# Kernel tuning notes

Hardware: AMD Instinct MI355X
Metric: run time of the kernel (lower is better)

Reference implementation:

```python
import jax, jax.numpy as jnp
import numpy as np

NUM_ITERATIONS = 100
EPS = 1e-6
LIPSCHITZ_COEFF = 0.9


def _l2_normalize(x, axis=None, eps=1e-12):
    return x * jax.lax.rsqrt((x * x).sum(axis=axis, keepdims=True) + eps)


def setup_inputs() -> dict:
    key = jax.random.key(0)
    k1, k2, k3, k4 = jax.random.split(key, 4)
    B, D_in, D_out = 32768, 1024, 1024
    x = jax.random.normal(k1, (B, D_in), dtype=jnp.float32)
    # TruncatedNormal(stddev=1/sqrt(fan_in)) approximated by scaled normal
    w = jax.random.normal(k2, (D_in, D_out), dtype=jnp.float32) / np.sqrt(D_in)
    b = jax.random.normal(k3, (D_out,), dtype=jnp.float32)
    u0 = jax.random.normal(k4, (1, D_out), dtype=jnp.float32)
    return {"x": x, "w": w, "b": b, "u0": u0}


def reference(x, w, b, u0):
    d_in = w.shape[0]

    # 100-step power iteration: tight sequential dependency chain of GEMV pairs.
    def body(i, carry):
        u, _ = carry
        v = _l2_normalize(jnp.matmul(u, w.T), eps=EPS)   # [1, d_in]
        u = _l2_normalize(jnp.matmul(v, w), eps=EPS)     # [1, d_out]
        return (u, v)

    v_init = jnp.zeros((1, d_in), dtype=w.dtype)
    u, v = jax.lax.fori_loop(0, NUM_ITERATIONS, body, (u0, v_init))
    u = jax.lax.stop_gradient(u)
    v = jax.lax.stop_gradient(v)

    sigma = jnp.matmul(jnp.matmul(v, w), u.T)[0, 0]      # spectral norm estimate
    factor = jnp.maximum(1.0, sigma / LIPSCHITZ_COEFF)
    w_norm = w / factor

    out = jnp.dot(x, w_norm) + b
    return out
```

## Files before the change

kernel.cpp:

```cpp
#include <hip/hip_runtime.h>
#include <hip/hip_bf16.h>
#include <cstdint>
#include <cstddef>

#define DDIM 1024
#define BROWS 32768

typedef __attribute__((ext_vector_type(8))) short short8;
typedef __attribute__((ext_vector_type(4))) float floatx4;

__device__ __forceinline__ float bf2f(unsigned short u) {
  return __uint_as_float(((unsigned int)u) << 16);
}
__device__ __forceinline__ unsigned short f2bf(float f) {
  unsigned int u = __float_as_uint(f);
  u += 0x7FFFu + ((u >> 16) & 1u);
  return (unsigned short)(u >> 16);
}

__device__ __forceinline__ void load_lds16(const void* g, void* l) {
  __builtin_amdgcn_global_load_lds(
      (const __attribute__((address_space(1))) unsigned int*)g,
      (__attribute__((address_space(3))) unsigned int*)l,
      16, 0, 0);
}

__global__ void __launch_bounds__(256, 2)
big_gemm(const float* __restrict__ Af, const unsigned short* __restrict__ Bt,
         float* __restrict__ Outf, const float* __restrict__ inv_ptr,
         const float* __restrict__ bias)
{
  __shared__ unsigned short As[128 * 32];
  __shared__ unsigned short Bs[128 * 32];

  const int tid  = threadIdx.x;
  const int lane = tid & 63;
  const int wid  = tid >> 6;
  const int wr = wid >> 1, wc = wid & 1;
  const int g = lane >> 4, r = lane & 15;

  const int bm0 = (int)(blockIdx.x & 255) * 128;
  const int bn0 = (int)(blockIdx.x >> 8) * 128;

  const floatx4 zero4 = {0.f, 0.f, 0.f, 0.f};
  floatx4 acc[4][4];
#pragma unroll
  for (int m = 0; m < 4; ++m)
#pragma unroll
    for (int n = 0; n < 4; ++n) acc[m][n] = zero4;

  for (int kk = 0; kk < DDIM; kk += 32) {
    __syncthreads();
#pragma unroll
    for (int p = 0; p < 2; ++p) {
      const int o = p * 4096 + tid * 16;
      const int row = o >> 6;
      const int cole = (o & 63) >> 1;
      load_lds16(Bt + (size_t)(bn0 + row) * DDIM + kk + cole, (char*)Bs + o);
    }
#pragma unroll
    for (int p = 0; p < 2; ++p) {
      const int o = p * 4096 + tid * 16;
      const int row = o >> 6;
      const int cole = (o & 63) >> 1;
      const float4* s = (const float4*)(Af + (size_t)(bm0 + row) * DDIM + kk + cole);
      float4 x0 = s[0], x1 = s[1];
      short8 t;
      t[0] = (short)f2bf(x0.x); t[1] = (short)f2bf(x0.y);
      t[2] = (short)f2bf(x0.z); t[3] = (short)f2bf(x0.w);
      t[4] = (short)f2bf(x1.x); t[5] = (short)f2bf(x1.y);
      t[6] = (short)f2bf(x1.z); t[7] = (short)f2bf(x1.w);
      *(short8*)((char*)As + o) = t;
    }
    __syncthreads();

    short8 afr[4], bfr[4];
#pragma unroll
    for (int m = 0; m < 4; ++m)
      afr[m] = *(const short8*)((const char*)As + (wr * 64 + m * 16 + r) * 64 + g * 16);
#pragma unroll
    for (int n = 0; n < 4; ++n)
      bfr[n] = *(const short8*)((const char*)Bs + (wc * 64 + n * 16 + r) * 64 + g * 16);
#pragma unroll
    for (int m = 0; m < 4; ++m)
#pragma unroll
      for (int n = 0; n < 4; ++n)
        acc[m][n] = __builtin_amdgcn_mfma_f32_16x16x32_bf16(afr[m], bfr[n], acc[m][n], 0, 0, 0);
  }

  const float inv = *inv_ptr;
#pragma unroll
  for (int n = 0; n < 4; ++n) {
    const int ocol = bn0 + wc * 64 + n * 16 + r;
    const float bv = bias[ocol];
#pragma unroll
    for (int m = 0; m < 4; ++m) {
      const int orow0 = bm0 + wr * 64 + m * 16 + g * 4;
#pragma unroll
      for (int q = 0; q < 4; ++q) {
        Outf[(size_t)(orow0 + q) * DDIM + ocol] = acc[m][n][q] * inv + bv;
      }
    }
  }
}

__global__ void __launch_bounds__(256, 2)
sq_gemm(const unsigned short* __restrict__ A, const unsigned short* __restrict__ Bt,
        unsigned short* __restrict__ Out, const float* __restrict__ in_max,
        float* __restrict__ out_max)
{
  __shared__ __align__(16) unsigned short As[2][4096];
  __shared__ __align__(16) unsigned short Bs[2][4096];
  __shared__ float redw[4];

  const int tid  = threadIdx.x;
  const int lane = tid & 63;
  const int wid  = tid >> 6;
  const int wr = wid >> 1, wc = wid & 1;
  const int g = lane >> 4, r = lane & 15;

  const int bm0 = (int)(blockIdx.x >> 4) * 64;
  const int bn0 = (int)(blockIdx.x & 15) * 64;

  const int so    = tid * 16;
  const int srow0 = so >> 7;
  const int sc16  = (so >> 4) & 7;
  const int scs   = sc16 ^ (srow0 & 7);
  const unsigned short* aSrc0 = A  + (size_t)(bm0 + srow0) * DDIM + scs * 8;
  const unsigned short* aSrc1 = A  + (size_t)(bm0 + 32 + srow0) * DDIM + scs * 8;
  const unsigned short* bSrc0 = Bt + (size_t)(bn0 + srow0) * DDIM + scs * 8;
  const unsigned short* bSrc1 = Bt + (size_t)(bn0 + 32 + srow0) * DDIM + scs * 8;

  const floatx4 zero4 = {0.f, 0.f, 0.f, 0.f};
  floatx4 acc[2][2];
#pragma unroll
  for (int fm = 0; fm < 2; ++fm)
#pragma unroll
    for (int fn = 0; fn < 2; ++fn) acc[fm][fn] = zero4;

  load_lds16(aSrc0, (char*)&As[0][0] + so);
  load_lds16(aSrc1, (char*)&As[0][0] + 4096 + so);
  load_lds16(bSrc0, (char*)&Bs[0][0] + so);
  load_lds16(bSrc1, (char*)&Bs[0][0] + 4096 + so);
  __syncthreads();

  int buf = 0;
  for (int t = 0; t < 16; ++t) {
    if (t + 1 < 16) {
      const int kk = (t + 1) * 64;
      load_lds16(aSrc0 + kk, (char*)&As[buf ^ 1][0] + so);
      load_lds16(aSrc1 + kk, (char*)&As[buf ^ 1][0] + 4096 + so);
      load_lds16(bSrc0 + kk, (char*)&Bs[buf ^ 1][0] + so);
      load_lds16(bSrc1 + kk, (char*)&Bs[buf ^ 1][0] + 4096 + so);
    }
#pragma unroll
    for (int ks = 0; ks < 2; ++ks) {
      const int chunk = ((ks << 2) + g) ^ (r & 7);
      short8 af[2], bf[2];
#pragma unroll
      for (int fm = 0; fm < 2; ++fm) {
        const int arow = wr * 32 + fm * 16 + r;
        af[fm] = *(const short8*)((const char*)&As[buf][0] + (arow << 7) + (chunk << 4));
      }
#pragma unroll
      for (int fn = 0; fn < 2; ++fn) {
        const int brow = wc * 32 + fn * 16 + r;
        bf[fn] = *(const short8*)((const char*)&Bs[buf][0] + (brow << 7) + (chunk << 4));
      }
#pragma unroll
      for (int fm = 0; fm < 2; ++fm)
#pragma unroll
        for (int fn = 0; fn < 2; ++fn)
          acc[fm][fn] = __builtin_amdgcn_mfma_f32_16x16x32_bf16(af[fm], bf[fn], acc[fm][fn], 0, 0, 0);
    }
    __syncthreads();
    buf ^= 1;
  }

  float c = 1.0f;
  if (in_max != nullptr) {
    int e;
    (void)frexpf(*in_max, &e);
    c = ldexpf(1.0f, -e);
  }
  const float c2 = c * c;
  float lmax = 0.0f;
#pragma unroll
  for (int fm = 0; fm < 2; ++fm) {
#pragma unroll
    for (int fn = 0; fn < 2; ++fn) {
      const int ocol = bn0 + wc * 32 + fn * 16 + r;
#pragma unroll
      for (int q = 0; q < 4; ++q) {
        const int orow = bm0 + wr * 32 + fm * 16 + g * 4 + q;
        float v = acc[fm][fn][q] * c2;
        Out[(size_t)orow * DDIM + ocol] = f2bf(v);
        lmax = fmaxf(lmax, fabsf(v));
      }
    }
  }
#pragma unroll
  for (int off = 32; off > 0; off >>= 1) lmax = fmaxf(lmax, __shfl_down(lmax, off));
  if (lane == 0) redw[wid] = lmax;
  __syncthreads();
  if (tid == 0) {
    float m = fmaxf(fmaxf(redw[0], redw[1]), fmaxf(redw[2], redw[3]));
    atomicMax((unsigned int*)out_max, __float_as_uint(m));
  }
}

__global__ void __launch_bounds__(256)
transpose_bf16(const float* __restrict__ W, unsigned short* __restrict__ WT)
{
  __shared__ float tile[64][65];
  const int bx = blockIdx.x & 15;
  const int by = blockIdx.x >> 4;
  const int tid = threadIdx.x;
  const int c = tid & 63;
  const int r0 = tid >> 6;
#pragma unroll
  for (int p = 0; p < 16; ++p) {
    int kr = p * 4 + r0;
    tile[kr][c] = W[(size_t)(bx * 64 + kr) * DDIM + by * 64 + c];
  }
  __syncthreads();
#pragma unroll
  for (int p = 0; p < 16; ++p) {
    int nr = p * 4 + r0;
    WT[(size_t)(by * 64 + nr) * DDIM + bx * 64 + c] = f2bf(tile[c][nr]);
  }
}

__global__ void __launch_bounds__(256)
gemv_pow(const unsigned short* __restrict__ P, const float* __restrict__ vin,
         float* __restrict__ vout)
{
  const int tid = threadIdx.x;
  const int lane = tid & 63;
  const int wid = tid >> 6;
  float vs[16];
  const float4* vv = (const float4*)(vin + lane * 16);
#pragma unroll
  for (int i = 0; i < 4; ++i) {
    float4 t = vv[i];
    vs[i * 4 + 0] = t.x; vs[i * 4 + 1] = t.y; vs[i * 4 + 2] = t.z; vs[i * 4 + 3] = t.w;
  }
#pragma unroll
  for (int rr = 0; rr < 4; ++rr) {
    const int row = (int)blockIdx.x * 16 + wid * 4 + rr;
    const unsigned short* pr = P + (size_t)row * DDIM + lane * 16;
    short8 p0 = *(const short8*)pr;
    short8 p1 = *(const short8*)(pr + 8);
    float s = 0.f;
#pragma unroll
    for (int e = 0; e < 8; ++e) s += bf2f((unsigned short)p0[e]) * vs[e];
#pragma unroll
    for (int e = 0; e < 8; ++e) s += bf2f((unsigned short)p1[e]) * vs[8 + e];
#pragma unroll
    for (int off = 32; off > 0; off >>= 1) s += __shfl_down(s, off);
    if (lane == 0) vout[row] = s * 0x1p-12f;
  }
}

__global__ void __launch_bounds__(256)
v_kernel(const float* __restrict__ W, const float* __restrict__ d,
         float* __restrict__ v_un, float* __restrict__ vpart)
{
  __shared__ float wsum[4];
  const int tid = threadIdx.x;
  const int lane = tid & 63;
  const int wid = tid >> 6;
  float vs[16];
  const float4* dv = (const float4*)(d + lane * 16);
#pragma unroll
  for (int i = 0; i < 4; ++i) {
    float4 t = dv[i];
    vs[i * 4 + 0] = t.x; vs[i * 4 + 1] = t.y; vs[i * 4 + 2] = t.z; vs[i * 4 + 3] = t.w;
  }
  float ssq = 0.f;
#pragma unroll
  for (int rr = 0; rr < 4; ++rr) {
    const int row = (int)blockIdx.x * 16 + wid * 4 + rr;
    const float4* wrow = (const float4*)(W + (size_t)row * DDIM + lane * 16);
    float s = 0.f;
#pragma unroll
    for (int i = 0; i < 4; ++i) {
      float4 t = wrow[i];
      s += t.x * vs[i * 4 + 0] + t.y * vs[i * 4 + 1] + t.z * vs[i * 4 + 2] + t.w * vs[i * 4 + 3];
    }
#pragma unroll
    for (int off = 32; off > 0; off >>= 1) s += __shfl_down(s, off);
    if (lane == 0) { v_un[row] = s; ssq += s * s; }
  }
  if (lane == 0) wsum[wid] = ssq;
  __syncthreads();
  if (tid == 0) vpart[blockIdx.x] = (wsum[0] + wsum[1]) + (wsum[2] + wsum[3]);
}

__global__ void __launch_bounds__(256)
t_fin_kernel(const float* __restrict__ W, const float* __restrict__ v_un,
             float* __restrict__ vpart, float* __restrict__ tpart,
             unsigned int* __restrict__ counter, float* __restrict__ inv_out)
{
  __shared__ float part[8][33];
  __shared__ unsigned int sticket;
  const int tid = threadIdx.x;
  const int col = (int)blockIdx.x * 32 + (tid & 31);
  const int ch = tid >> 5;
  float s = 0.f;
  const int i0 = ch * 128;
  for (int i = i0; i < i0 + 128; ++i)
    s += v_un[i] * W[(size_t)i * DDIM + col];
  part[ch][tid & 31] = s;
  __syncthreads();
  if (tid < 32) {
    float t = 0.f;
#pragma unroll
    for (int c2 = 0; c2 < 8; ++c2) t += part[c2][tid];
    part[0][tid] = t * t;
  }
  __syncthreads();
  if (tid == 0) {
    float ss = 0.f;
#pragma unroll
    for (int c = 0; c < 32; ++c) ss += part[0][c];
    tpart[blockIdx.x] = ss;
    __threadfence();
    sticket = atomicAdd(counter, 1u);
  }
  __syncthreads();
  if (sticket == 31) {
    __threadfence();
    float val = 0.f;
    if (tid < 64)
      val = __uint_as_float(atomicOr((unsigned int*)&vpart[tid], 0u));
    part[tid >> 5][tid & 31] = val;
    __syncthreads();
    if (tid == 0) {
      float sv = 0.f;
      for (int i = 0; i < 64; ++i) sv += part[i >> 5][i & 31];
      float stq = 0.f;
      for (int i = 0; i < 32; ++i)
        stq += __uint_as_float(atomicOr((unsigned int*)&tpart[i], 0u));
      float sigma = sqrtf(stq / sv);
      inv_out[0] = (sigma > 0.9f) ? (0.9f / sigma) : 1.0f;
    }
  }
}

extern "C" void kernel_launch(void* const* d_in, const int* in_sizes, int n_in,
                              void* d_out, int out_size, void* d_ws, size_t ws_size,
                              hipStream_t stream)
{
  const float* x  = (const float*)d_in[0];
  const float* w  = (const float*)d_in[1];
  const float* b  = (const float*)d_in[2];
  const float* u0 = (const float*)d_in[3];
  float* out = (float*)d_out;

  char* ws = (char*)d_ws;
  float* scal = (float*)ws;
  float* u_a  = (float*)(ws + 0x1000);
  float* u_b  = (float*)(ws + 0x2000);
  float* v_un = (float*)(ws + 0x3000);
  unsigned short* WT = (unsigned short*)(ws + 0x4000);
  unsigned short* P0 = (unsigned short*)(ws + 0x204000);
  unsigned short* P1 = (unsigned short*)(ws + 0x404000);

  hipMemsetAsync(d_ws, 0, 4096, stream);
  hipLaunchKernelGGL(transpose_bf16, dim3(256), dim3(256), 0, stream, w, WT);

  hipLaunchKernelGGL(sq_gemm, dim3(256), dim3(256), 0, stream,
                     WT, WT, P0, (const float*)nullptr, &scal[0]);
  hipLaunchKernelGGL(sq_gemm, dim3(256), dim3(256), 0, stream,
                     P0, P0, P1, &scal[0], &scal[1]);
  hipLaunchKernelGGL(sq_gemm, dim3(256), dim3(256), 0, stream,
                     P1, P1, P0, &scal[1], &scal[2]);
  hipLaunchKernelGGL(sq_gemm, dim3(256), dim3(256), 0, stream,
                     P0, P0, P1, &scal[2], &scal[3]);
  hipLaunchKernelGGL(sq_gemm, dim3(256), dim3(256), 0, stream,
                     P1, P1, P0, &scal[3], &scal[4]);
  hipLaunchKernelGGL(sq_gemm, dim3(256), dim3(256), 0, stream,
                     P0, P0, P1, &scal[4], &scal[5]);

  hipLaunchKernelGGL(gemv_pow, dim3(64), dim3(256), 0, stream, P1, u0, u_a);
  hipLaunchKernelGGL(gemv_pow, dim3(64), dim3(256), 0, stream, P1, u_a, u_b);
  hipLaunchKernelGGL(gemv_pow, dim3(64), dim3(256), 0, stream, P1, u_b, u_a);

  hipLaunchKernelGGL(v_kernel, dim3(64), dim3(256), 0, stream, w, u_a, v_un, &scal[16]);
  hipLaunchKernelGGL(t_fin_kernel, dim3(32), dim3(256), 0, stream,
                     w, v_un, &scal[16], &scal[80],
                     (unsigned int*)&scal[120], &scal[8]);

  hipLaunchKernelGGL(big_gemm, dim3(2048), dim3(256), 0, stream,
                     x, WT, out, &scal[8], b);
}
```

Baseline: 253.9 us.

## Prefetch x into cache using extra blocks in squaring GEMM launches

Each sq_gemm launch gets 256 extra blocks that stream slices of x (float4 reads summed into a sink) and do no matrix work. Across the six launches these blocks cover the whole 128MB x tensor. The goal is to use idle bandwidth during the latency-bound repeated squaring phase to warm the last-level cache before big_gemm reads x. The risk is that x is larger than the MI355X Infinity Cache, so most prefetched lines may be evicted, and the extra blocks compete with the GEMM blocks for CUs and memory bandwidth.

```diff
diff --git a/kernel.cpp b/kernel.cpp
--- a/kernel.cpp
+++ b/kernel.cpp
@@ -107,13 +107,30 @@
 __global__ void __launch_bounds__(256, 2)
 sq_gemm(const unsigned short* __restrict__ A, const unsigned short* __restrict__ Bt,
         unsigned short* __restrict__ Out, const float* __restrict__ in_max,
-        float* __restrict__ out_max)
+        float* __restrict__ out_max,
+        const float* __restrict__ warm, float* __restrict__ warm_sink, int slot0)
 {
   __shared__ __align__(16) unsigned short As[2][4096];
   __shared__ __align__(16) unsigned short Bs[2][4096];
   __shared__ float redw[4];
 
   const int tid  = threadIdx.x;
+
+  if ((int)blockIdx.x >= 256) {
+    const int slot = slot0 + ((int)blockIdx.x - 256);
+    const long long base = (long long)slot * 21848;
+    long long end = base + 21848;
+    const long long N = (long long)BROWS * DDIM;
+    if (end > N) end = N;
+    float s = 0.f;
+    for (long long i = base + (tid << 2); i < end; i += 1024) {
+      float4 v = *(const float4*)(warm + i);
+      s += v.x + v.y + v.z + v.w;
+    }
+    warm_sink[slot & 63] = s;
+    return;
+  }
+
   const int lane = tid & 63;
   const int wid  = tid >> 6;
   const int wr = wid >> 1, wc = wid & 1;
@@ -360,6 +377,7 @@
 
   char* ws = (char*)d_ws;
   float* scal = (float*)ws;
+  float* wsink = (float*)(ws + 0x800);
   float* u_a  = (float*)(ws + 0x1000);
   float* u_b  = (float*)(ws + 0x2000);
   float* v_un = (float*)(ws + 0x3000);
@@ -370,18 +388,19 @@
   hipMemsetAsync(d_ws, 0, 4096, stream);
   hipLaunchKernelGGL(transpose_bf16, dim3(256), dim3(256), 0, stream, w, WT);
 
-  hipLaunchKernelGGL(sq_gemm, dim3(256), dim3(256), 0, stream,
-                     WT, WT, P0, (const float*)nullptr, &scal[0]);
-  hipLaunchKernelGGL(sq_gemm, dim3(256), dim3(256), 0, stream,
-                     P0, P0, P1, &scal[0], &scal[1]);
-  hipLaunchKernelGGL(sq_gemm, dim3(256), dim3(256), 0, stream,
-                     P1, P1, P0, &scal[1], &scal[2]);
-  hipLaunchKernelGGL(sq_gemm, dim3(256), dim3(256), 0, stream,
-                     P0, P0, P1, &scal[2], &scal[3]);
-  hipLaunchKernelGGL(sq_gemm, dim3(256), dim3(256), 0, stream,
-                     P1, P1, P0, &scal[3], &scal[4]);
-  hipLaunchKernelGGL(sq_gemm, dim3(256), dim3(256), 0, stream,
-                     P0, P0, P1, &scal[4], &scal[5]);
+  hipLaunchKernelGGL(sq_gemm, dim3(512), dim3(256), 0, stream,
+                     WT, WT, P0, (const float*)nullptr, &scal[0],
+                     x, wsink, 0);
+  hipLaunchKernelGGL(sq_gemm, dim3(512), dim3(256), 0, stream,
+                     P0, P0, P1, &scal[0], &scal[1], x, wsink, 256);
+  hipLaunchKernelGGL(sq_gemm, dim3(512), dim3(256), 0, stream,
+                     P1, P1, P0, &scal[1], &scal[2], x, wsink, 512);
+  hipLaunchKernelGGL(sq_gemm, dim3(512), dim3(256), 0, stream,
+                     P0, P0, P1, &scal[2], &scal[3], x, wsink, 768);
+  hipLaunchKernelGGL(sq_gemm, dim3(512), dim3(256), 0, stream,
+                     P1, P1, P0, &scal[3], &scal[4], x, wsink, 1024);
+  hipLaunchKernelGGL(sq_gemm, dim3(512), dim3(256), 0, stream,
+                     P0, P0, P1, &scal[4], &scal[5], x, wsink, 1280);
 
   hipLaunchKernelGGL(gemv_pow, dim3(64), dim3(256), 0, stream, P1, u0, u_a);
   hipLaunchKernelGGL(gemv_pow, dim3(64), dim3(256), 0, stream, P1, u_a, u_b);
```

Result: no change. 258.4 us (+1.8%).

## Prefetch x into cache using idle blocks of the small GEMV kernels

Applied to the files above, without the earlier changes.

Adds extra blocks to the gemv_pow, v_kernel and t_fin_kernel launches. These blocks stream slices of x (the 128 MB activation matrix) and sum them into a sink buffer, so x is warm in the last-level cache before big_gemm reads it. This tries to hide part of big_gemm's memory traffic behind the latency-bound power-iteration chain. The risks are bandwidth contention that slows the small kernels, and the fact that only about 100 MB of x can stay resident, so part of the prefetch may be evicted.

```diff
diff --git a/kernel.cpp b/kernel.cpp
--- a/kernel.cpp
+++ b/kernel.cpp
@@ -23,6 +23,22 @@
       (const __attribute__((address_space(1))) unsigned int*)g,
       (__attribute__((address_space(3))) unsigned int*)l,
       16, 0, 0);
+}
+
+__device__ __forceinline__ void do_warm(const float* __restrict__ warm,
+                                        float* __restrict__ sink,
+                                        int slot, int tid)
+{
+  const long long base = (long long)slot * 33856;
+  long long end = base + 33856;
+  const long long N = (long long)BROWS * DDIM;
+  if (end > N) end = N;
+  float s = 0.f;
+  for (long long i = base + (tid << 2); i < end; i += 1024) {
+    float4 v = *(const float4*)(warm + i);
+    s += v.x + v.y + v.z + v.w;
+  }
+  sink[slot & 63] = s;
 }
 
 __global__ void __launch_bounds__(256, 2)
@@ -233,9 +249,14 @@
 
 __global__ void __launch_bounds__(256)
 gemv_pow(const unsigned short* __restrict__ P, const float* __restrict__ vin,
-         float* __restrict__ vout)
+         float* __restrict__ vout,
+         const float* __restrict__ warm, float* __restrict__ wsink, int slot0)
 {
   const int tid = threadIdx.x;
+  if ((int)blockIdx.x >= 64) {
+    do_warm(warm, wsink, slot0 + ((int)blockIdx.x - 64), tid);
+    return;
+  }
   const int lane = tid & 63;
   const int wid = tid >> 6;
   float vs[16];
@@ -264,10 +285,15 @@
 
 __global__ void __launch_bounds__(256)
 v_kernel(const float* __restrict__ W, const float* __restrict__ d,
-         float* __restrict__ v_un, float* __restrict__ vpart)
+         float* __restrict__ v_un, float* __restrict__ vpart,
+         const float* __restrict__ warm, float* __restrict__ wsink, int slot0)
 {
   __shared__ float wsum[4];
   const int tid = threadIdx.x;
+  if ((int)blockIdx.x >= 64) {
+    do_warm(warm, wsink, slot0 + ((int)blockIdx.x - 64), tid);
+    return;
+  }
   const int lane = tid & 63;
   const int wid = tid >> 6;
   float vs[16];
@@ -300,11 +326,16 @@
 __global__ void __launch_bounds__(256)
 t_fin_kernel(const float* __restrict__ W, const float* __restrict__ v_un,
              float* __restrict__ vpart, float* __restrict__ tpart,
-             unsigned int* __restrict__ counter, float* __restrict__ inv_out)
+             unsigned int* __restrict__ counter, float* __restrict__ inv_out,
+             const float* __restrict__ warm, float* __restrict__ wsink, int slot0)
 {
   __shared__ float part[8][33];
   __shared__ unsigned int sticket;
   const int tid = threadIdx.x;
+  if ((int)blockIdx.x >= 32) {
+    do_warm(warm, wsink, slot0 + ((int)blockIdx.x - 32), tid);
+    return;
+  }
   const int col = (int)blockIdx.x * 32 + (tid & 31);
   const int ch = tid >> 5;
   float s = 0.f;
@@ -360,6 +391,7 @@
 
   char* ws = (char*)d_ws;
   float* scal = (float*)ws;
+  float* wsink = (float*)(ws + 0x800);
   float* u_a  = (float*)(ws + 0x1000);
   float* u_b  = (float*)(ws + 0x2000);
   float* v_un = (float*)(ws + 0x3000);
@@ -383,14 +415,18 @@
   hipLaunchKernelGGL(sq_gemm, dim3(256), dim3(256), 0, stream,
                      P0, P0, P1, &scal[4], &scal[5]);
 
-  hipLaunchKernelGGL(gemv_pow, dim3(64), dim3(256), 0, stream, P1, u0, u_a);
-  hipLaunchKernelGGL(gemv_pow, dim3(64), dim3(256), 0, stream, P1, u_a, u_b);
-  hipLaunchKernelGGL(gemv_pow, dim3(64), dim3(256), 0, stream, P1, u_b, u_a);
-
-  hipLaunchKernelGGL(v_kernel, dim3(64), dim3(256), 0, stream, w, u_a, v_un, &scal[16]);
-  hipLaunchKernelGGL(t_fin_kernel, dim3(32), dim3(256), 0, stream,
+  hipLaunchKernelGGL(gemv_pow, dim3(256), dim3(256), 0, stream,
+                     P1, u0, u_a, x, wsink, 0);
+  hipLaunchKernelGGL(gemv_pow, dim3(256), dim3(256), 0, stream,
+                     P1, u_a, u_b, x, wsink, 192);
+  hipLaunchKernelGGL(gemv_pow, dim3(256), dim3(256), 0, stream,
+                     P1, u_b, u_a, x, wsink, 384);
+
+  hipLaunchKernelGGL(v_kernel, dim3(256), dim3(256), 0, stream,
+                     w, u_a, v_un, &scal[16], x, wsink, 576);
+  hipLaunchKernelGGL(t_fin_kernel, dim3(256), dim3(256), 0, stream,
                      w, v_un, &scal[16], &scal[80],
-                     (unsigned int*)&scal[120], &scal[8]);
+                     (unsigned int*)&scal[120], &scal[8], x, wsink, 768);
 
   hipLaunchKernelGGL(big_gemm, dim3(2048), dim3(256), 0, stream,
                      x, WT, out, &scal[8], b);
```

Measured after the change: 287.0 us. +13.0%, slower.
